# Performance work log

Hardware: AMD Instinct MI355X
Metric: run time of the kernel (lower is better)

The kernel has to match this reference:

```python
import jax, jax.numpy as jnp
import numpy as np

NH, DH = 16, 64          # n_head, d_head
CH = NH + DH             # 80
RQ, RK, RV = 6, 2, 2
ROPE_BASE = 10000.0


def _rotary(b, cache_len):
    # b: [B, T, R, DH]; rotates the d-factor exactly as the torch Rotary module
    T = b.shape[1]
    inv_freq = (1.0 / ROPE_BASE) ** (jnp.arange(0, DH, 2, dtype=jnp.float32) / DH)
    t = jnp.arange(T, dtype=jnp.float32) + cache_len
    freqs = jnp.outer(t, inv_freq)                      # [T, DH/2]
    cos = freqs[None, :, None, :].astype(b.dtype)
    sin = jnp.sin(freqs)[None, :, None, :].astype(b.dtype)
    cos = jnp.cos(freqs)[None, :, None, :].astype(b.dtype)
    x1, x2 = jnp.split(b, 2, axis=3)
    return jnp.concatenate([x1 * cos + x2 * sin, -x1 * sin + x2 * cos], axis=3)


def setup_inputs() -> dict:
    key = jax.random.key(0)
    k1, k2, k3, k4 = jax.random.split(key, 4)
    B, T, D = 2, 2048, 1024
    x = jax.random.normal(k1, (B, T, D), dtype=jnp.float32)
    # xavier-uniform-like scale for factor projections
    s_q = float(np.sqrt(6.0 / (D + CH)))
    s_o = float(np.sqrt(6.0 / (D + D)))
    W_abq = jax.random.uniform(k2, (RQ * CH, D), minval=-s_q, maxval=s_q, dtype=jnp.float32)
    W_abkv = jax.random.uniform(k3, ((RK + RV) * CH, D), minval=-s_q, maxval=s_q, dtype=jnp.float32)
    W_o = jax.random.uniform(k4, (D, D), minval=-s_o, maxval=s_o, dtype=jnp.float32)
    return {"x": x, "W_abq": W_abq, "W_abkv": W_abkv, "W_o": W_o}


def reference(x, W_abq, W_abkv, W_o):
    B, T, D = x.shape
    # low-rank factor projections
    abq = (x @ W_abq.T).reshape(B, T, RQ, CH)
    a_q, b_q = abq[..., :NH], abq[..., NH:]            # [B,T,RQ,NH], [B,T,RQ,DH]
    abkv = (x @ W_abkv.T).reshape(B, T, RK + RV, CH)
    a_kv = abkv[..., :NH]
    b_kv = _rotary(abkv[..., NH:], cache_len=0)        # RoPE applied to K/V d-factors only
    a_k, b_k = a_kv[:, :, :RK], b_kv[:, :, :RK]
    a_v, b_v = a_kv[:, :, RK:], b_kv[:, :, RK:]
    # tensor-product reconstruction of Q/K/V
    q = jnp.einsum('btrh,btrd->bthd', a_q, b_q) / RQ
    k = jnp.einsum('btrh,btrd->bthd', a_k, b_k) / RK
    v = jnp.einsum('btrh,btrd->bthd', a_v, b_v) / RV
    # causal attention (flex_attention default scale = 1/sqrt(dh))
    scale = 1.0 / jnp.sqrt(jnp.asarray(DH, dtype=q.dtype))
    scores = jnp.einsum('bqhd,bkhd->bhqk', q, k) * scale
    causal = jnp.tril(jnp.ones((T, T), dtype=bool))
    scores = jnp.where(causal[None, None], scores, jnp.finfo(scores.dtype).min)
    attn = jax.nn.softmax(scores, axis=-1)
    y = jnp.einsum('bhqk,bkhd->bqhd', attn, v).reshape(B, T, D)
    return y @ W_o.T
```

## Files before the change

### kernel.cpp

```cpp
#include <hip/hip_runtime.h>
#include <hip/hip_bf16.h>
#include <math.h>

#define NHEADS 16
#define DHEAD  64
#define CHDIM  80
#define RQn    6
#define RKn    2
#define RVn    2
#define BB     2
#define TT     2048
#define DDim   1024
#define NQK    800

using frag16 = __attribute__((ext_vector_type(8))) short;
using f32x4  = __attribute__((ext_vector_type(4))) float;
using f32x16 = __attribute__((ext_vector_type(16))) float;

#define AS1(p) ((const __attribute__((address_space(1))) unsigned int*)(p))
#define AS3(p) ((__attribute__((address_space(3))) unsigned int*)(p))

static __device__ __forceinline__ unsigned short bf16_bits(float f) {
    __hip_bfloat16 h = __float2bfloat16(f);
    return *(unsigned short*)&h;
}
static __device__ __forceinline__ unsigned int pk2(float a, float b) {
    return ((unsigned int)bf16_bits(b) << 16) | (unsigned int)bf16_bits(a);
}

__global__ __launch_bounds__(256) void cvt_all(
    const float* __restrict__ x, const float* __restrict__ wq,
    const float* __restrict__ wk, const float* __restrict__ wo,
    __hip_bfloat16* __restrict__ xb, __hip_bfloat16* __restrict__ wqk,
    __hip_bfloat16* __restrict__ wob)
{
    int bid = blockIdx.x;
    const float* src; __hip_bfloat16* dst; int n4;
    if (bid < 4096)      { src = x;  dst = xb;            n4 = 1048576; }
    else if (bid < 4576) { bid -= 4096; src = wq; dst = wqk;           n4 = 122880; }
    else if (bid < 4896) { bid -= 4576; src = wk; dst = wqk + 491520;  n4 = 81920; }
    else                 { bid -= 4896; src = wo; dst = wob;           n4 = 262144; }
    int i = bid * 256 + threadIdx.x;
    if (i < n4) {
        float4 v = *(const float4*)&src[i * 4];
        ushort4 o;
        o.x = bf16_bits(v.x); o.y = bf16_bits(v.y);
        o.z = bf16_bits(v.z); o.w = bf16_bits(v.w);
        *(ushort4*)&dst[i * 4] = o;
    }
}

__global__ __launch_bounds__(256) void gemm_bf16(
    const __hip_bfloat16* __restrict__ A, const __hip_bfloat16* __restrict__ W,
    float* __restrict__ C, int M, int N, int K)
{
    __shared__ __hip_bfloat16 Asl[2][64 * 64];
    __shared__ __hip_bfloat16 Bsl[2][128 * 64];
    const int tid = threadIdx.x;
    const int w = tid >> 6, lane = tid & 63;
    const int l16 = lane & 15, quad = lane >> 4;
    const int bm = blockIdx.y * 64, bn = blockIdx.x * 128;

    int rSA[2], cSA[2];
    #pragma unroll
    for (int j = 0; j < 2; j++) {
        int L = (w * 2 + j) * 64 + lane;
        rSA[j] = L >> 3;
        cSA[j] = (L & 7) ^ (rSA[j] & 7);
    }
    int rSB[4], cSB[4];
    #pragma unroll
    for (int j = 0; j < 4; j++) {
        int L = (w * 4 + j) * 64 + lane;
        int r = L >> 3;
        cSB[j] = (L & 7) ^ (r & 7);
        int rb = bn + r;
        rSB[j] = (rb < N) ? rb : (N - 1);
    }

    f32x4 acc[4][2];
    #pragma unroll
    for (int mt = 0; mt < 4; mt++)
        #pragma unroll
        for (int nt = 0; nt < 2; nt++)
            acc[mt][nt] = (f32x4){0.f, 0.f, 0.f, 0.f};

    const int nK = K >> 6;
    #pragma unroll
    for (int j = 0; j < 2; j++)
        __builtin_amdgcn_global_load_lds(AS1(A + (size_t)(bm + rSA[j]) * K + cSA[j] * 8),
                                         AS3(&Asl[0][(w * 2 + j) * 512]), 16, 0, 0);
    #pragma unroll
    for (int j = 0; j < 4; j++)
        __builtin_amdgcn_global_load_lds(AS1(W + (size_t)rSB[j] * K + cSB[j] * 8),
                                         AS3(&Bsl[0][(w * 4 + j) * 512]), 16, 0, 0);

    for (int kk = 0; kk < nK; kk++) {
        const int cur = kk & 1;
        __syncthreads();
        if (kk + 1 < nK) {
            const int k1 = (kk + 1) * 64;
            #pragma unroll
            for (int j = 0; j < 2; j++)
                __builtin_amdgcn_global_load_lds(AS1(A + (size_t)(bm + rSA[j]) * K + k1 + cSA[j] * 8),
                                                 AS3(&Asl[cur ^ 1][(w * 2 + j) * 512]), 16, 0, 0);
            #pragma unroll
            for (int j = 0; j < 4; j++)
                __builtin_amdgcn_global_load_lds(AS1(W + (size_t)rSB[j] * K + k1 + cSB[j] * 8),
                                                 AS3(&Bsl[cur ^ 1][(w * 4 + j) * 512]), 16, 0, 0);
        }
        #pragma unroll
        for (int ks = 0; ks < 2; ks++) {
            frag16 af[4], bf[2];
            #pragma unroll
            for (int mt = 0; mt < 4; mt++) {
                int r = mt * 16 + l16;
                af[mt] = *(const frag16*)&Asl[cur][r * 64 + (((ks * 4 + quad) ^ (r & 7)) * 8)];
            }
            #pragma unroll
            for (int nt = 0; nt < 2; nt++) {
                int r = w * 32 + nt * 16 + l16;
                bf[nt] = *(const frag16*)&Bsl[cur][r * 64 + (((ks * 4 + quad) ^ (r & 7)) * 8)];
            }
            #pragma unroll
            for (int mt = 0; mt < 4; mt++)
                #pragma unroll
                for (int nt = 0; nt < 2; nt++)
                    acc[mt][nt] = __builtin_amdgcn_mfma_f32_16x16x32_bf16(af[mt], bf[nt], acc[mt][nt], 0, 0, 0);
        }
    }
    #pragma unroll
    for (int mt = 0; mt < 4; mt++) {
        #pragma unroll
        for (int reg = 0; reg < 4; reg++) {
            int row = bm + mt * 16 + quad * 4 + reg;
            #pragma unroll
            for (int nt = 0; nt < 2; nt++) {
                int col = bn + w * 32 + nt * 16 + l16;
                if (col < N) C[(size_t)row * N + col] = acc[mt][nt][reg];
            }
        }
    }
}

__global__ __launch_bounds__(256) void qkv_kernel(
    const float* __restrict__ ab,
    __hip_bfloat16* __restrict__ q, __hip_bfloat16* __restrict__ k,
    __hip_bfloat16* __restrict__ vT)
{
    const int tok0 = blockIdx.x * 4;
    const int w = threadIdx.x >> 6;
    const int d = threadIdx.x & 63;
    const int token = tok0 + w;
    const int b = token / TT;
    const int t = token % TT;
    __shared__ float sq[4][RQn * CHDIM];
    __shared__ float skv[4][(RKn + RVn) * CHDIM];
    __shared__ __align__(8) __hip_bfloat16 vbuf[NHEADS][DHEAD][4];
    const float* aq  = ab + (size_t)token * NQK;
    const float* akv = aq + 480;
    for (int i = d; i < RQn * CHDIM; i += 64) sq[w][i] = aq[i];
    for (int i = d; i < (RKn + RVn) * CHDIM; i += 64) skv[w][i] = akv[i];
    const int i32 = d & 31;
    float inv_freq = powf(10000.0f, -(float)i32 / 32.0f);
    float fr = (float)t * inv_freq;
    float c = cosf(fr), s = sinf(fr);
    float rot[4];
    #pragma unroll
    for (int r = 0; r < 4; r++) {
        float x1 = skv[w][r * CHDIM + NHEADS + i32];
        float x2 = skv[w][r * CHDIM + NHEADS + 32 + i32];
        rot[r] = (d < 32) ? (x1 * c + x2 * s) : (-x1 * s + x2 * c);
    }
    float bqv[RQn];
    #pragma unroll
    for (int r = 0; r < RQn; r++) bqv[r] = sq[w][r * CHDIM + NHEADS + d];
    #pragma unroll
    for (int h = 0; h < NHEADS; h++) {
        float accq = 0.0f;
        #pragma unroll
        for (int r = 0; r < RQn; r++)
            accq += sq[w][r * CHDIM + h] * bqv[r];
        q[((size_t)(b * NHEADS + h) * TT + t) * DHEAD + d] = __float2bfloat16(accq * (0.125f / 6.0f));
        float acck = 0.0f, accv = 0.0f;
        #pragma unroll
        for (int r = 0; r < RKn; r++)
            acck += skv[w][r * CHDIM + h] * rot[r];
        #pragma unroll
        for (int r = 0; r < RVn; r++)
            accv += skv[w][(RKn + r) * CHDIM + h] * rot[RKn + r];
        k[((size_t)(b * NHEADS + h) * TT + t) * DHEAD + d] = __float2bfloat16(acck * 0.5f);
        vbuf[h][d][w] = __float2bfloat16(accv * 0.5f);
    }
    __syncthreads();
    const int t0 = tok0 % TT;
    const int b0 = tok0 / TT;
    for (int row = threadIdx.x; row < NHEADS * DHEAD; row += 256) {
        int h = row >> 6, dd = row & 63;
        *(uint2*)&vT[((size_t)(b0 * NHEADS + h) * DHEAD + dd) * TT + t0] =
            *(const uint2*)&vbuf[h][dd][0];
    }
}

static __device__ __forceinline__ void build_pfrag(
    const float* s0, const float* s1, frag16 Pf[4], const int hi, const int paddr)
{
    #pragma unroll
    for (int k2 = 0; k2 < 4; k2++) {
        const float* sF = (k2 >= 2) ? s1 : s0;
        const int bs = 8 * (k2 & 1);
        unsigned int u0a = pk2(sF[bs + 0], sF[bs + 1]);
        unsigned int u0b = pk2(sF[bs + 2], sF[bs + 3]);
        unsigned int u1a = pk2(sF[bs + 4], sF[bs + 5]);
        unsigned int u1b = pk2(sF[bs + 6], sF[bs + 7]);
        unsigned int r0a = (unsigned int)__builtin_amdgcn_ds_bpermute(paddr, (int)u0a);
        unsigned int r0b = (unsigned int)__builtin_amdgcn_ds_bpermute(paddr, (int)u0b);
        unsigned int r1a = (unsigned int)__builtin_amdgcn_ds_bpermute(paddr, (int)u1a);
        unsigned int r1b = (unsigned int)__builtin_amdgcn_ds_bpermute(paddr, (int)u1b);
        union { frag16 f; unsigned int u[4]; } pf;
        pf.u[0] = hi ? r1a : u0a;
        pf.u[1] = hi ? r1b : u0b;
        pf.u[2] = hi ? u1a : r0a;
        pf.u[3] = hi ? u1b : r0b;
        Pf[k2] = pf.f;
    }
}

static __device__ __forceinline__ void attn_tile(
    const __hip_bfloat16* __restrict__ Kc, const __hip_bfloat16* __restrict__ Vc,
    const frag16 qB[4], f32x16& O0, f32x16& O1, float& lpart,
    const int l31, const int hi, const int xi, const int paddr,
    const bool domask, const int kb0, const int qlane)
{
    f32x16 ST0 = {}, ST1 = {};
    #pragma unroll
    for (int kt4 = 0; kt4 < 4; kt4++) {
        int c8 = kt4 * 2 + hi;
        frag16 kf0 = *(const frag16*)&Kc[l31 * 64 + ((c8 ^ xi) * 8)];
        frag16 kf1 = *(const frag16*)&Kc[(32 + l31) * 64 + ((c8 ^ xi) * 8)];
        ST0 = __builtin_amdgcn_mfma_f32_32x32x16_bf16(kf0, qB[kt4], ST0, 0, 0, 0);
        ST1 = __builtin_amdgcn_mfma_f32_32x32x16_bf16(kf1, qB[kt4], ST1, 0, 0, 0);
    }
    float* s0 = (float*)&ST0;
    float* s1 = (float*)&ST1;
    if (domask) {
        int kbq = kb0 + 4 * hi;
        #pragma unroll
        for (int reg = 0; reg < 16; reg++) {
            int rowc = (reg & 3) + 8 * (reg >> 2);
            if (kbq + rowc > qlane)      s0[reg] = -1e30f;
            if (kbq + 32 + rowc > qlane) s1[reg] = -1e30f;
        }
    }
    #pragma unroll
    for (int reg = 0; reg < 16; reg++) {
        float p0 = __expf(s0[reg]);
        float p1 = __expf(s1[reg]);
        s0[reg] = p0; s1[reg] = p1;
        lpart += p0 + p1;
    }
    frag16 Pf[4];
    build_pfrag(s0, s1, Pf, hi, paddr);
    #pragma unroll
    for (int k2 = 0; k2 < 4; k2++) {
        int c8 = k2 * 2 + hi;
        frag16 vf0 = *(const frag16*)&Vc[l31 * 64 + ((c8 ^ xi) * 8)];
        frag16 vf1 = *(const frag16*)&Vc[(32 + l31) * 64 + ((c8 ^ xi) * 8)];
        O0 = __builtin_amdgcn_mfma_f32_32x32x16_bf16(vf0, Pf[k2], O0, 0, 0, 0);
        O1 = __builtin_amdgcn_mfma_f32_32x32x16_bf16(vf1, Pf[k2], O1, 0, 0, 0);
    }
}

static __device__ __forceinline__ void attn_tile2(
    const __hip_bfloat16* __restrict__ Kc, const __hip_bfloat16* __restrict__ Vc,
    const frag16 qBlo[4], const frag16 qBhi[4],
    f32x16& Olo0, f32x16& Olo1, float& l_lo,
    f32x16& Ohi0, f32x16& Ohi1, float& l_hi,
    const int l31, const int hi, const int xi, const int paddr,
    const bool domask_lo, const int kb0, const int qlane_lo)
{
    f32x16 SL0 = {}, SL1 = {}, SH0 = {}, SH1 = {};
    #pragma unroll
    for (int kt4 = 0; kt4 < 4; kt4++) {
        int c8 = kt4 * 2 + hi;
        frag16 kf0 = *(const frag16*)&Kc[l31 * 64 + ((c8 ^ xi) * 8)];
        frag16 kf1 = *(const frag16*)&Kc[(32 + l31) * 64 + ((c8 ^ xi) * 8)];
        SL0 = __builtin_amdgcn_mfma_f32_32x32x16_bf16(kf0, qBlo[kt4], SL0, 0, 0, 0);
        SH0 = __builtin_amdgcn_mfma_f32_32x32x16_bf16(kf0, qBhi[kt4], SH0, 0, 0, 0);
        SL1 = __builtin_amdgcn_mfma_f32_32x32x16_bf16(kf1, qBlo[kt4], SL1, 0, 0, 0);
        SH1 = __builtin_amdgcn_mfma_f32_32x32x16_bf16(kf1, qBhi[kt4], SH1, 0, 0, 0);
    }
    float* sl0 = (float*)&SL0; float* sl1 = (float*)&SL1;
    float* sh0 = (float*)&SH0; float* sh1 = (float*)&SH1;
    if (domask_lo) {
        int kbq = kb0 + 4 * hi;
        #pragma unroll
        for (int reg = 0; reg < 16; reg++) {
            int rowc = (reg & 3) + 8 * (reg >> 2);
            if (kbq + rowc > qlane_lo)      sl0[reg] = -1e30f;
            if (kbq + 32 + rowc > qlane_lo) sl1[reg] = -1e30f;
        }
    }
    #pragma unroll
    for (int reg = 0; reg < 16; reg++) {
        float a = __expf(sl0[reg]); float b = __expf(sl1[reg]);
        float c = __expf(sh0[reg]); float d = __expf(sh1[reg]);
        sl0[reg] = a; sl1[reg] = b; sh0[reg] = c; sh1[reg] = d;
        l_lo += a + b; l_hi += c + d;
    }
    frag16 PfL[4], PfH[4];
    build_pfrag(sl0, sl1, PfL, hi, paddr);
    build_pfrag(sh0, sh1, PfH, hi, paddr);
    #pragma unroll
    for (int k2 = 0; k2 < 4; k2++) {
        int c8 = k2 * 2 + hi;
        frag16 vf0 = *(const frag16*)&Vc[l31 * 64 + ((c8 ^ xi) * 8)];
        frag16 vf1 = *(const frag16*)&Vc[(32 + l31) * 64 + ((c8 ^ xi) * 8)];
        Olo0 = __builtin_amdgcn_mfma_f32_32x32x16_bf16(vf0, PfL[k2], Olo0, 0, 0, 0);
        Ohi0 = __builtin_amdgcn_mfma_f32_32x32x16_bf16(vf0, PfH[k2], Ohi0, 0, 0, 0);
        Olo1 = __builtin_amdgcn_mfma_f32_32x32x16_bf16(vf1, PfL[k2], Olo1, 0, 0, 0);
        Ohi1 = __builtin_amdgcn_mfma_f32_32x32x16_bf16(vf1, PfH[k2], Ohi1, 0, 0, 0);
    }
}

__global__ __launch_bounds__(256, 2) void flash_mfma(
    const __hip_bfloat16* __restrict__ q, const __hip_bfloat16* __restrict__ k,
    const __hip_bfloat16* __restrict__ vT, __hip_bfloat16* __restrict__ y,
    float* __restrict__ Op, float* __restrict__ Lp)
{
    const int g = blockIdx.x;
    const int bh = g & 31;
    const int pr = g >> 5;
    const int qthalf = pr & 7;
    const int part = pr >> 3;
    const int qt_lo = qthalf, qt_hi = 15 - qthalf;
    const int nlo = 2 * qt_lo + 2;
    const int S = 17 - nlo;
    const int b = bh >> 4, h = bh & 15;
    const int tid = threadIdx.x;
    const int w = tid >> 6;
    const int lane = tid & 63;
    const int l31 = lane & 31;
    const int hi = lane >> 5;
    const int xi = l31 & 7;
    const int paddr = (lane ^ 32) << 2;

    __shared__ __align__(16) __hip_bfloat16 KsF[2][4096];
    __shared__ __align__(16) __hip_bfloat16 VsF[2][4096];

    const size_t base = (size_t)bh * TT * DHEAD;
    const __hip_bfloat16* qb = q + base;
    const __hip_bfloat16* kb = k + base;
    const __hip_bfloat16* vb = vT + base;

    const int ktd_lo = 2 * qt_lo + (w >> 1);
    const int ktd_hi = 2 * qt_hi + (w >> 1);
    const int qlane_lo = qt_lo * 128 + w * 32 + l31;
    const int qlane_hi = qt_hi * 128 + w * 32 + l31;

    const int k0off  = part ? S : 0;
    const int nsteps = part ? 17 : ((nlo > S) ? nlo : S);

    int offK[2], offV[2];
    #pragma unroll
    for (int j = 0; j < 2; j++) {
        int Lc = w * 128 + j * 64 + lane;
        int r = Lc >> 3, c8 = Lc & 7, g8 = c8 ^ (r & 7);
        offK[j] = r * 64 + g8 * 8;
        offV[j] = r * TT + g8 * 8;
    }

    frag16 qB_hi[4], qB_lo[4];
    #pragma unroll
    for (int kt4 = 0; kt4 < 4; kt4++)
        qB_hi[kt4] = *(const frag16*)&qb[(size_t)qlane_hi * DHEAD + kt4 * 16 + hi * 8];
    if (part == 0) {
        #pragma unroll
        for (int kt4 = 0; kt4 < 4; kt4++)
            qB_lo[kt4] = *(const frag16*)&qb[(size_t)qlane_lo * DHEAD + kt4 * 16 + hi * 8];
    }

    f32x16 Olo0 = {}, Olo1 = {}, Ohi0 = {}, Ohi1 = {};
    float l_lo = 0.0f, l_hi = 0.0f;

    #pragma unroll
    for (int j = 0; j < 2; j++) {
        __builtin_amdgcn_global_load_lds(AS1(kb + (size_t)k0off * 4096 + offK[j]),
                                         AS3(&KsF[0][w * 1024 + j * 512]), 16, 0, 0);
        __builtin_amdgcn_global_load_lds(AS1(vb + (size_t)k0off * 64 + offV[j]),
                                         AS3(&VsF[0][w * 1024 + j * 512]), 16, 0, 0);
    }

    for (int kt = 0; kt < nsteps; kt++) {
        const int cur = kt & 1;
        __syncthreads();
        if (kt + 1 < nsteps) {
            const int phys1 = k0off + kt + 1;
            #pragma unroll
            for (int j = 0; j < 2; j++) {
                __builtin_amdgcn_global_load_lds(AS1(kb + (size_t)phys1 * 4096 + offK[j]),
                                                 AS3(&KsF[cur ^ 1][w * 1024 + j * 512]), 16, 0, 0);
                __builtin_amdgcn_global_load_lds(AS1(vb + (size_t)phys1 * 64 + offV[j]),
                                                 AS3(&VsF[cur ^ 1][w * 1024 + j * 512]), 16, 0, 0);
            }
        }
        const __hip_bfloat16* Kc = KsF[cur];
        const __hip_bfloat16* Vc = VsF[cur];
        if (part == 0) {
            const bool do_lo = (kt <= ktd_lo);
            const bool do_hi = (kt < S);
            if (do_lo && do_hi)
                attn_tile2(Kc, Vc, qB_lo, qB_hi, Olo0, Olo1, l_lo, Ohi0, Ohi1, l_hi,
                           l31, hi, xi, paddr, kt == ktd_lo, kt * 64, qlane_lo);
            else if (do_lo)
                attn_tile(Kc, Vc, qB_lo, Olo0, Olo1, l_lo, l31, hi, xi, paddr,
                          kt == ktd_lo, kt * 64, qlane_lo);
            else if (do_hi)
                attn_tile(Kc, Vc, qB_hi, Ohi0, Ohi1, l_hi, l31, hi, xi, paddr,
                          false, 0, qlane_hi);
        } else {
            const int phys = S + kt;
            if (phys <= ktd_hi)
                attn_tile(Kc, Vc, qB_hi, Ohi0, Ohi1, l_hi, l31, hi, xi, paddr,
                          phys == ktd_hi, phys * 64, qlane_hi);
        }
    }

    if (part == 0) {
        float lother = __int_as_float(__builtin_amdgcn_ds_bpermute(paddr, __float_as_int(l_lo)));
        float inv = 1.0f / (l_lo + lother);
        float* o0 = (float*)&Olo0;
        float* o1 = (float*)&Olo1;
        __hip_bfloat16* yp = y + ((size_t)(b * TT + qlane_lo)) * DDim + h * DHEAD;
        #pragma unroll
        for (int gg = 0; gg < 4; gg++) {
            int d0 = 8 * gg + 4 * hi;
            uint2 pa, pb;
            pa.x = pk2(o0[4*gg+0] * inv, o0[4*gg+1] * inv);
            pa.y = pk2(o0[4*gg+2] * inv, o0[4*gg+3] * inv);
            pb.x = pk2(o1[4*gg+0] * inv, o1[4*gg+1] * inv);
            pb.y = pk2(o1[4*gg+2] * inv, o1[4*gg+3] * inv);
            *(uint2*)&yp[d0] = pa;
            *(uint2*)&yp[32 + d0] = pb;
        }
    }
    {
        float lother = __int_as_float(__builtin_amdgcn_ds_bpermute(paddr, __float_as_int(l_hi)));
        float ltot = l_hi + lother;
        const int slot = bh * 8 + qthalf;
        const int rloc = w * 32 + l31;
        float* Od = Op + ((size_t)part * 256 + slot) * 8192 + (size_t)rloc * 64;
        float* o0 = (float*)&Ohi0;
        float* o1 = (float*)&Ohi1;
        #pragma unroll
        for (int gg = 0; gg < 4; gg++) {
            int d0 = 8 * gg + 4 * hi;
            *(float4*)&Od[d0]      = (float4){o0[4*gg+0], o0[4*gg+1], o0[4*gg+2], o0[4*gg+3]};
            *(float4*)&Od[32 + d0] = (float4){o1[4*gg+0], o1[4*gg+1], o1[4*gg+2], o1[4*gg+3]};
        }
        if (hi == 0) Lp[part * 32768 + slot * 128 + rloc] = ltot;
    }
}

__global__ __launch_bounds__(256) void combine(
    const float* __restrict__ Op, const float* __restrict__ Lp,
    __hip_bfloat16* __restrict__ y)
{
    int idx = blockIdx.x * 256 + threadIdx.x;
    int slot = idx >> 7, row = idx & 127;
    int bh = slot >> 3, qthalf = slot & 7;
    int b = bh >> 4, h = bh & 15;
    int qrow = (15 - qthalf) * 128 + row;
    float l0 = Lp[slot * 128 + row];
    float l1 = Lp[32768 + slot * 128 + row];
    float inv = 1.0f / (l0 + l1);
    const float* p0 = Op + (size_t)(slot * 128 + row) * 64;
    const float* p1 = p0 + 2097152;
    __hip_bfloat16* yp = y + ((size_t)(b * TT + qrow)) * DDim + h * DHEAD;
    #pragma unroll
    for (int c = 0; c < 64; c += 8) {
        float4 a0 = *(const float4*)&p0[c];
        float4 a1 = *(const float4*)&p0[c + 4];
        float4 b0 = *(const float4*)&p1[c];
        float4 b1 = *(const float4*)&p1[c + 4];
        uint4 o;
        o.x = pk2((a0.x + b0.x) * inv, (a0.y + b0.y) * inv);
        o.y = pk2((a0.z + b0.z) * inv, (a0.w + b0.w) * inv);
        o.z = pk2((a1.x + b1.x) * inv, (a1.y + b1.y) * inv);
        o.w = pk2((a1.z + b1.z) * inv, (a1.w + b1.w) * inv);
        *(uint4*)&yp[c] = o;
    }
}

extern "C" void kernel_launch(void* const* d_in, const int* in_sizes, int n_in,
                              void* d_out, int out_size, void* d_ws, size_t ws_size,
                              hipStream_t stream) {
    const float* x      = (const float*)d_in[0];
    const float* W_abq  = (const float*)d_in[1];
    const float* W_abkv = (const float*)d_in[2];
    const float* W_o    = (const float*)d_in[3];
    float* out = (float*)d_out;

    char* ws = (char*)d_ws;
    __hip_bfloat16* xb   = (__hip_bfloat16*)ws;  ws += (size_t)4194304 * 2;
    __hip_bfloat16* wqk  = (__hip_bfloat16*)ws;  ws += (size_t)NQK * 1024 * 2;
    __hip_bfloat16* wo_b = (__hip_bfloat16*)ws;  ws += (size_t)1048576 * 2;
    float* abqkv = (float*)ws;                   ws += (size_t)4096 * NQK * 4;
    __hip_bfloat16* qb = (__hip_bfloat16*)ws;    ws += (size_t)4194304 * 2;
    __hip_bfloat16* kb = (__hip_bfloat16*)ws;    ws += (size_t)4194304 * 2;
    __hip_bfloat16* vT = (__hip_bfloat16*)ws;    ws += (size_t)4194304 * 2;
    __hip_bfloat16* yb = (__hip_bfloat16*)ws;    ws += (size_t)4194304 * 2;
    float* Op = (float*)ws;                      ws += (size_t)2 * 2097152 * 4;
    float* Lp = (float*)ws;                      ws += (size_t)2 * 32768 * 4;

    cvt_all<<<dim3(5920), dim3(256), 0, stream>>>(x, W_abq, W_abkv, W_o, xb, wqk, wo_b);
    gemm_bf16<<<dim3(7, 64), dim3(256), 0, stream>>>(xb, wqk, abqkv, 4096, NQK, 1024);
    qkv_kernel<<<dim3(1024), dim3(256), 0, stream>>>(abqkv, qb, kb, vT);
    flash_mfma<<<dim3(512), dim3(256), 0, stream>>>(qb, kb, vT, yb, Op, Lp);
    combine<<<dim3(128), dim3(256), 0, stream>>>(Op, Lp, yb);
    gemm_bf16<<<dim3(8, 64), dim3(256), 0, stream>>>(yb, wo_b, out, 4096, 1024, 1024);
}
```

Before: 176.7 us.

## Fuse convert, QKV projection GEMM and QKV build into persistent kernel with grid barriers

Merges the conversion, first GEMM and QKV reconstruction kernels into one persistent 512-block kernel separated by atomic-counter grid barriers, with a memset to reset the counters each call. This removes two kernel launches and their inter-kernel gaps. It also removes the dual-tile attention path in flash_mfma, so the lo and hi query tiles are processed by separate attn_tile calls. The grid barrier relies on all 512 blocks being co-resident, uses system-scope fences and spinning, and adds a memset launch.

```diff
diff --git a/kernel.cpp b/kernel.cpp
--- a/kernel.cpp
+++ b/kernel.cpp
@@ -8,10 +8,10 @@
 #define RQn    6
 #define RKn    2
 #define RVn    2
-#define BB     2
 #define TT     2048
 #define DDim   1024
 #define NQK    800
+#define GRID   512
 
 using frag16 = __attribute__((ext_vector_type(8))) short;
 using f32x4  = __attribute__((ext_vector_type(4))) float;
@@ -28,26 +28,205 @@
     return ((unsigned int)bf16_bits(b) << 16) | (unsigned int)bf16_bits(a);
 }
 
-__global__ __launch_bounds__(256) void cvt_all(
+static __device__ __forceinline__ void gbar(unsigned* cell) {
+    __syncthreads();
+    if (threadIdx.x == 0) {
+        __builtin_amdgcn_s_waitcnt(0);
+        __threadfence_system();
+        __builtin_amdgcn_s_waitcnt(0);
+        __hip_atomic_fetch_add(cell, 1u, __ATOMIC_SEQ_CST, __HIP_MEMORY_SCOPE_SYSTEM);
+        while (__hip_atomic_load(cell, __ATOMIC_SEQ_CST, __HIP_MEMORY_SCOPE_SYSTEM) < (unsigned)GRID)
+            __builtin_amdgcn_s_sleep(2);
+        __threadfence_system();
+        __builtin_amdgcn_s_waitcnt(0);
+    }
+    __syncthreads();
+}
+
+static __device__ void dev_gemm(const __hip_bfloat16* __restrict__ A,
+                                const __hip_bfloat16* __restrict__ W,
+                                float* __restrict__ C,
+                                int N, int K, int bm, int bn, char* smem)
+{
+    __hip_bfloat16* Asl = (__hip_bfloat16*)smem;
+    __hip_bfloat16* Bsl = (__hip_bfloat16*)(smem + 16384);
+    const int tid = threadIdx.x;
+    const int w = tid >> 6, lane = tid & 63;
+    const int l16 = lane & 15, quad = lane >> 4;
+
+    int rSA[2], cSA[2];
+    #pragma unroll
+    for (int j = 0; j < 2; j++) {
+        int L = (w * 2 + j) * 64 + lane;
+        rSA[j] = L >> 3;
+        cSA[j] = (L & 7) ^ (rSA[j] & 7);
+    }
+    int rSB[4], cSB[4];
+    #pragma unroll
+    for (int j = 0; j < 4; j++) {
+        int L = (w * 4 + j) * 64 + lane;
+        int r = L >> 3;
+        cSB[j] = (L & 7) ^ (r & 7);
+        int rb = bn + r;
+        rSB[j] = (rb < N) ? rb : (N - 1);
+    }
+
+    f32x4 acc[4][2];
+    #pragma unroll
+    for (int mt = 0; mt < 4; mt++)
+        #pragma unroll
+        for (int nt = 0; nt < 2; nt++)
+            acc[mt][nt] = (f32x4){0.f, 0.f, 0.f, 0.f};
+
+    const int nK = K >> 6;
+    #pragma unroll
+    for (int j = 0; j < 2; j++)
+        __builtin_amdgcn_global_load_lds(AS1(A + (size_t)(bm + rSA[j]) * K + cSA[j] * 8),
+                                         AS3(&Asl[(w * 2 + j) * 512]), 16, 0, 0);
+    #pragma unroll
+    for (int j = 0; j < 4; j++)
+        __builtin_amdgcn_global_load_lds(AS1(W + (size_t)rSB[j] * K + cSB[j] * 8),
+                                         AS3(&Bsl[(w * 4 + j) * 512]), 16, 0, 0);
+
+    for (int kk = 0; kk < nK; kk++) {
+        const int cur = kk & 1;
+        __syncthreads();
+        if (kk + 1 < nK) {
+            const int k1 = (kk + 1) * 64;
+            #pragma unroll
+            for (int j = 0; j < 2; j++)
+                __builtin_amdgcn_global_load_lds(AS1(A + (size_t)(bm + rSA[j]) * K + k1 + cSA[j] * 8),
+                                                 AS3(&Asl[(cur ^ 1) * 4096 + (w * 2 + j) * 512]), 16, 0, 0);
+            #pragma unroll
+            for (int j = 0; j < 4; j++)
+                __builtin_amdgcn_global_load_lds(AS1(W + (size_t)rSB[j] * K + k1 + cSB[j] * 8),
+                                                 AS3(&Bsl[(cur ^ 1) * 8192 + (w * 4 + j) * 512]), 16, 0, 0);
+        }
+        #pragma unroll
+        for (int ks = 0; ks < 2; ks++) {
+            frag16 af[4], bf[2];
+            #pragma unroll
+            for (int mt = 0; mt < 4; mt++) {
+                int r = mt * 16 + l16;
+                af[mt] = *(const frag16*)&Asl[cur * 4096 + r * 64 + (((ks * 4 + quad) ^ (r & 7)) * 8)];
+            }
+            #pragma unroll
+            for (int nt = 0; nt < 2; nt++) {
+                int r = w * 32 + nt * 16 + l16;
+                bf[nt] = *(const frag16*)&Bsl[cur * 8192 + r * 64 + (((ks * 4 + quad) ^ (r & 7)) * 8)];
+            }
+            #pragma unroll
+            for (int mt = 0; mt < 4; mt++)
+                #pragma unroll
+                for (int nt = 0; nt < 2; nt++)
+                    acc[mt][nt] = __builtin_amdgcn_mfma_f32_16x16x32_bf16(af[mt], bf[nt], acc[mt][nt], 0, 0, 0);
+        }
+    }
+    #pragma unroll
+    for (int mt = 0; mt < 4; mt++) {
+        #pragma unroll
+        for (int reg = 0; reg < 4; reg++) {
+            int row = bm + mt * 16 + quad * 4 + reg;
+            #pragma unroll
+            for (int nt = 0; nt < 2; nt++) {
+                int col = bn + w * 32 + nt * 16 + l16;
+                if (col < N) C[(size_t)row * N + col] = acc[mt][nt][reg];
+            }
+        }
+    }
+}
+
+static __device__ void dev_qkv(const float* __restrict__ ab,
+                               __hip_bfloat16* __restrict__ q, __hip_bfloat16* __restrict__ k,
+                               __hip_bfloat16* __restrict__ vT, int vb, char* smem)
+{
+    float* sq  = (float*)smem;
+    float* skv = (float*)(smem + 7680);
+    __hip_bfloat16* vbuf = (__hip_bfloat16*)(smem + 12800);
+    __syncthreads();
+    const int tok0 = vb * 4;
+    const int w = threadIdx.x >> 6;
+    const int d = threadIdx.x & 63;
+    const int token = tok0 + w;
+    const int b = token / TT;
+    const int t = token % TT;
+    const float* aq  = ab + (size_t)token * NQK;
+    const float* akv = aq + 480;
+    for (int i = d; i < RQn * CHDIM; i += 64) sq[w * 480 + i] = aq[i];
+    for (int i = d; i < (RKn + RVn) * CHDIM; i += 64) skv[w * 320 + i] = akv[i];
+    const int i32 = d & 31;
+    float inv_freq = powf(10000.0f, -(float)i32 / 32.0f);
+    float fr = (float)t * inv_freq;
+    float c = cosf(fr), s = sinf(fr);
+    float rot[4];
+    #pragma unroll
+    for (int r = 0; r < 4; r++) {
+        float x1 = skv[w * 320 + r * CHDIM + NHEADS + i32];
+        float x2 = skv[w * 320 + r * CHDIM + NHEADS + 32 + i32];
+        rot[r] = (d < 32) ? (x1 * c + x2 * s) : (-x1 * s + x2 * c);
+    }
+    float bqv[RQn];
+    #pragma unroll
+    for (int r = 0; r < RQn; r++) bqv[r] = sq[w * 480 + r * CHDIM + NHEADS + d];
+    #pragma unroll
+    for (int h = 0; h < NHEADS; h++) {
+        float accq = 0.0f;
+        #pragma unroll
+        for (int r = 0; r < RQn; r++)
+            accq += sq[w * 480 + r * CHDIM + h] * bqv[r];
+        q[((size_t)(b * NHEADS + h) * TT + t) * DHEAD + d] = __float2bfloat16(accq * (0.125f / 6.0f));
+        float acck = 0.0f, accv = 0.0f;
+        #pragma unroll
+        for (int r = 0; r < RKn; r++)
+            acck += skv[w * 320 + r * CHDIM + h] * rot[r];
+        #pragma unroll
+        for (int r = 0; r < RVn; r++)
+            accv += skv[w * 320 + (RKn + r) * CHDIM + h] * rot[RKn + r];
+        k[((size_t)(b * NHEADS + h) * TT + t) * DHEAD + d] = __float2bfloat16(acck * 0.5f);
+        vbuf[(h * 64 + d) * 4 + w] = __float2bfloat16(accv * 0.5f);
+    }
+    __syncthreads();
+    const int t0 = tok0 % TT;
+    const int b0 = tok0 / TT;
+    for (int row = threadIdx.x; row < NHEADS * DHEAD; row += 256) {
+        int h = row >> 6, dd = row & 63;
+        *(uint2*)&vT[((size_t)(b0 * NHEADS + h) * DHEAD + dd) * TT + t0] =
+            *(const uint2*)&vbuf[(h * 64 + dd) * 4];
+    }
+}
+
+__global__ __launch_bounds__(256, 2) void front(
     const float* __restrict__ x, const float* __restrict__ wq,
     const float* __restrict__ wk, const float* __restrict__ wo,
     __hip_bfloat16* __restrict__ xb, __hip_bfloat16* __restrict__ wqk,
-    __hip_bfloat16* __restrict__ wob)
-{
-    int bid = blockIdx.x;
-    const float* src; __hip_bfloat16* dst; int n4;
-    if (bid < 4096)      { src = x;  dst = xb;            n4 = 1048576; }
-    else if (bid < 4576) { bid -= 4096; src = wq; dst = wqk;           n4 = 122880; }
-    else if (bid < 4896) { bid -= 4576; src = wk; dst = wqk + 491520;  n4 = 81920; }
-    else                 { bid -= 4896; src = wo; dst = wob;           n4 = 262144; }
-    int i = bid * 256 + threadIdx.x;
-    if (i < n4) {
-        float4 v = *(const float4*)&src[i * 4];
+    __hip_bfloat16* __restrict__ wob, float* __restrict__ abqkv,
+    __hip_bfloat16* __restrict__ qb, __hip_bfloat16* __restrict__ kb,
+    __hip_bfloat16* __restrict__ vT, unsigned* __restrict__ cnt)
+{
+    __shared__ __align__(16) char smem[49152];
+    const int g = blockIdx.x;
+    const int tid = threadIdx.x;
+
+    for (int i = g * 256 + tid; i < 1515520; i += GRID * 256) {
+        const float* src; __hip_bfloat16* dst; int off;
+        if (i < 1048576)      { src = x;  dst = xb;           off = i; }
+        else if (i < 1171456) { src = wq; dst = wqk;          off = i - 1048576; }
+        else if (i < 1253376) { src = wk; dst = wqk + 491520; off = i - 1171456; }
+        else                  { src = wo; dst = wob;          off = i - 1253376; }
+        float4 v = *(const float4*)&src[(size_t)off * 4];
         ushort4 o;
         o.x = bf16_bits(v.x); o.y = bf16_bits(v.y);
         o.z = bf16_bits(v.z); o.w = bf16_bits(v.w);
-        *(ushort4*)&dst[i * 4] = o;
-    }
+        *(ushort4*)&dst[(size_t)off * 4] = o;
+    }
+    gbar(&cnt[0]);
+
+    if (g < 448)
+        dev_gemm(xb, wqk, abqkv, NQK, 1024, (g / 7) * 64, (g % 7) * 128, smem);
+    gbar(&cnt[1]);
+
+    dev_qkv(abqkv, qb, kb, vT, g * 2 + 0, smem);
+    dev_qkv(abqkv, qb, kb, vT, g * 2 + 1, smem);
 }
 
 __global__ __launch_bounds__(256) void gemm_bf16(
@@ -140,65 +319,6 @@
                 if (col < N) C[(size_t)row * N + col] = acc[mt][nt][reg];
             }
         }
-    }
-}
-
-__global__ __launch_bounds__(256) void qkv_kernel(
-    const float* __restrict__ ab,
-    __hip_bfloat16* __restrict__ q, __hip_bfloat16* __restrict__ k,
-    __hip_bfloat16* __restrict__ vT)
-{
-    const int tok0 = blockIdx.x * 4;
-    const int w = threadIdx.x >> 6;
-    const int d = threadIdx.x & 63;
-    const int token = tok0 + w;
-    const int b = token / TT;
-    const int t = token % TT;
-    __shared__ float sq[4][RQn * CHDIM];
-    __shared__ float skv[4][(RKn + RVn) * CHDIM];
-    __shared__ __align__(8) __hip_bfloat16 vbuf[NHEADS][DHEAD][4];
-    const float* aq  = ab + (size_t)token * NQK;
-    const float* akv = aq + 480;
-    for (int i = d; i < RQn * CHDIM; i += 64) sq[w][i] = aq[i];
-    for (int i = d; i < (RKn + RVn) * CHDIM; i += 64) skv[w][i] = akv[i];
-    const int i32 = d & 31;
-    float inv_freq = powf(10000.0f, -(float)i32 / 32.0f);
-    float fr = (float)t * inv_freq;
-    float c = cosf(fr), s = sinf(fr);
-    float rot[4];
-    #pragma unroll
-    for (int r = 0; r < 4; r++) {
-        float x1 = skv[w][r * CHDIM + NHEADS + i32];
-        float x2 = skv[w][r * CHDIM + NHEADS + 32 + i32];
-        rot[r] = (d < 32) ? (x1 * c + x2 * s) : (-x1 * s + x2 * c);
-    }
-    float bqv[RQn];
-    #pragma unroll
-    for (int r = 0; r < RQn; r++) bqv[r] = sq[w][r * CHDIM + NHEADS + d];
-    #pragma unroll
-    for (int h = 0; h < NHEADS; h++) {
-        float accq = 0.0f;
-        #pragma unroll
-        for (int r = 0; r < RQn; r++)
-            accq += sq[w][r * CHDIM + h] * bqv[r];
-        q[((size_t)(b * NHEADS + h) * TT + t) * DHEAD + d] = __float2bfloat16(accq * (0.125f / 6.0f));
-        float acck = 0.0f, accv = 0.0f;
-        #pragma unroll
-        for (int r = 0; r < RKn; r++)
-            acck += skv[w][r * CHDIM + h] * rot[r];
-        #pragma unroll
-        for (int r = 0; r < RVn; r++)
-            accv += skv[w][(RKn + r) * CHDIM + h] * rot[RKn + r];
-        k[((size_t)(b * NHEADS + h) * TT + t) * DHEAD + d] = __float2bfloat16(acck * 0.5f);
-        vbuf[h][d][w] = __float2bfloat16(accv * 0.5f);
-    }
-    __syncthreads();
-    const int t0 = tok0 % TT;
-    const int b0 = tok0 / TT;
-    for (int row = threadIdx.x; row < NHEADS * DHEAD; row += 256) {
-        int h = row >> 6, dd = row & 63;
-        *(uint2*)&vT[((size_t)(b0 * NHEADS + h) * DHEAD + dd) * TT + t0] =
-            *(const uint2*)&vbuf[h][dd][0];
     }
 }
 
@@ -271,58 +391,6 @@
     }
 }
 
-static __device__ __forceinline__ void attn_tile2(
-    const __hip_bfloat16* __restrict__ Kc, const __hip_bfloat16* __restrict__ Vc,
-    const frag16 qBlo[4], const frag16 qBhi[4],
-    f32x16& Olo0, f32x16& Olo1, float& l_lo,
-    f32x16& Ohi0, f32x16& Ohi1, float& l_hi,
-    const int l31, const int hi, const int xi, const int paddr,
-    const bool domask_lo, const int kb0, const int qlane_lo)
-{
-    f32x16 SL0 = {}, SL1 = {}, SH0 = {}, SH1 = {};
-    #pragma unroll
-    for (int kt4 = 0; kt4 < 4; kt4++) {
-        int c8 = kt4 * 2 + hi;
-        frag16 kf0 = *(const frag16*)&Kc[l31 * 64 + ((c8 ^ xi) * 8)];
-        frag16 kf1 = *(const frag16*)&Kc[(32 + l31) * 64 + ((c8 ^ xi) * 8)];
-        SL0 = __builtin_amdgcn_mfma_f32_32x32x16_bf16(kf0, qBlo[kt4], SL0, 0, 0, 0);
-        SH0 = __builtin_amdgcn_mfma_f32_32x32x16_bf16(kf0, qBhi[kt4], SH0, 0, 0, 0);
-        SL1 = __builtin_amdgcn_mfma_f32_32x32x16_bf16(kf1, qBlo[kt4], SL1, 0, 0, 0);
-        SH1 = __builtin_amdgcn_mfma_f32_32x32x16_bf16(kf1, qBhi[kt4], SH1, 0, 0, 0);
-    }
-    float* sl0 = (float*)&SL0; float* sl1 = (float*)&SL1;
-    float* sh0 = (float*)&SH0; float* sh1 = (float*)&SH1;
-    if (domask_lo) {
-        int kbq = kb0 + 4 * hi;
-        #pragma unroll
-        for (int reg = 0; reg < 16; reg++) {
-            int rowc = (reg & 3) + 8 * (reg >> 2);
-            if (kbq + rowc > qlane_lo)      sl0[reg] = -1e30f;
-            if (kbq + 32 + rowc > qlane_lo) sl1[reg] = -1e30f;
-        }
-    }
-    #pragma unroll
-    for (int reg = 0; reg < 16; reg++) {
-        float a = __expf(sl0[reg]); float b = __expf(sl1[reg]);
-        float c = __expf(sh0[reg]); float d = __expf(sh1[reg]);
-        sl0[reg] = a; sl1[reg] = b; sh0[reg] = c; sh1[reg] = d;
-        l_lo += a + b; l_hi += c + d;
-    }
-    frag16 PfL[4], PfH[4];
-    build_pfrag(sl0, sl1, PfL, hi, paddr);
-    build_pfrag(sh0, sh1, PfH, hi, paddr);
-    #pragma unroll
-    for (int k2 = 0; k2 < 4; k2++) {
-        int c8 = k2 * 2 + hi;
-        frag16 vf0 = *(const frag16*)&Vc[l31 * 64 + ((c8 ^ xi) * 8)];
-        frag16 vf1 = *(const frag16*)&Vc[(32 + l31) * 64 + ((c8 ^ xi) * 8)];
-        Olo0 = __builtin_amdgcn_mfma_f32_32x32x16_bf16(vf0, PfL[k2], Olo0, 0, 0, 0);
-        Ohi0 = __builtin_amdgcn_mfma_f32_32x32x16_bf16(vf0, PfH[k2], Ohi0, 0, 0, 0);
-        Olo1 = __builtin_amdgcn_mfma_f32_32x32x16_bf16(vf1, PfL[k2], Olo1, 0, 0, 0);
-        Ohi1 = __builtin_amdgcn_mfma_f32_32x32x16_bf16(vf1, PfH[k2], Ohi1, 0, 0, 0);
-    }
-}
-
 __global__ __launch_bounds__(256, 2) void flash_mfma(
     const __hip_bfloat16* __restrict__ q, const __hip_bfloat16* __restrict__ k,
     const __hip_bfloat16* __restrict__ vT, __hip_bfloat16* __restrict__ y,
@@ -407,15 +475,10 @@
         const __hip_bfloat16* Kc = KsF[cur];
         const __hip_bfloat16* Vc = VsF[cur];
         if (part == 0) {
-            const bool do_lo = (kt <= ktd_lo);
-            const bool do_hi = (kt < S);
-            if (do_lo && do_hi)
-                attn_tile2(Kc, Vc, qB_lo, qB_hi, Olo0, Olo1, l_lo, Ohi0, Ohi1, l_hi,
-                           l31, hi, xi, paddr, kt == ktd_lo, kt * 64, qlane_lo);
-            else if (do_lo)
+            if (kt <= ktd_lo)
                 attn_tile(Kc, Vc, qB_lo, Olo0, Olo1, l_lo, l31, hi, xi, paddr,
                           kt == ktd_lo, kt * 64, qlane_lo);
-            else if (do_hi)
+            if (kt < S)
                 attn_tile(Kc, Vc, qB_hi, Ohi0, Ohi1, l_hi, l31, hi, xi, paddr,
                           false, 0, qlane_hi);
         } else {
@@ -502,6 +565,7 @@
     float* out = (float*)d_out;
 
     char* ws = (char*)d_ws;
+    unsigned* cnt = (unsigned*)ws;               ws += 256;
     __hip_bfloat16* xb   = (__hip_bfloat16*)ws;  ws += (size_t)4194304 * 2;
     __hip_bfloat16* wqk  = (__hip_bfloat16*)ws;  ws += (size_t)NQK * 1024 * 2;
     __hip_bfloat16* wo_b = (__hip_bfloat16*)ws;  ws += (size_t)1048576 * 2;
@@ -513,9 +577,9 @@
     float* Op = (float*)ws;                      ws += (size_t)2 * 2097152 * 4;
     float* Lp = (float*)ws;                      ws += (size_t)2 * 32768 * 4;
 
-    cvt_all<<<dim3(5920), dim3(256), 0, stream>>>(x, W_abq, W_abkv, W_o, xb, wqk, wo_b);
-    gemm_bf16<<<dim3(7, 64), dim3(256), 0, stream>>>(xb, wqk, abqkv, 4096, NQK, 1024);
-    qkv_kernel<<<dim3(1024), dim3(256), 0, stream>>>(abqkv, qb, kb, vT);
+    hipMemsetAsync(cnt, 0, 8 * sizeof(unsigned), stream);
+    front<<<dim3(GRID), dim3(256), 0, stream>>>(
+        x, W_abq, W_abkv, W_o, xb, wqk, wo_b, abqkv, qb, kb, vT, cnt);
     flash_mfma<<<dim3(512), dim3(256), 0, stream>>>(qb, kb, vT, yb, Op, Lp);
     combine<<<dim3(128), dim3(256), 0, stream>>>(Op, Lp, yb);
     gemm_bf16<<<dim3(8, 64), dim3(256), 0, stream>>>(yb, wo_b, out, 4096, 1024, 1024);
```

After: 323.5 us. 1.83x slower.

## Split paired causal attention work into four equal key-range parts per block

Applied to the files above, without the earlier changes.

Reorganizes the flash attention work split. Each (lo,hi) query-tile pair's 34 key steps are concatenated and divided into four roughly equal segments, one per block, giving 1024 blocks instead of 512, and the fused dual-tile path is dropped. Every partial result now goes to the Op/Lp workspace, and the combine kernel is rewritten to sum up to four partials per row, using four threads per row. Occupancy is raised to 4 blocks per CU through launch bounds. The aim is better load balance and more parallelism, at the cost of more partial-result traffic, a heavier combine, and losing the Q-fragment reuse the dual-tile path had.

```diff
diff --git a/kernel.cpp b/kernel.cpp
--- a/kernel.cpp
+++ b/kernel.cpp
@@ -8,7 +8,6 @@
 #define RQn    6
 #define RKn    2
 #define RVn    2
-#define BB     2
 #define TT     2048
 #define DDim   1024
 #define NQK    800
@@ -271,72 +270,22 @@
     }
 }
 
-static __device__ __forceinline__ void attn_tile2(
-    const __hip_bfloat16* __restrict__ Kc, const __hip_bfloat16* __restrict__ Vc,
-    const frag16 qBlo[4], const frag16 qBhi[4],
-    f32x16& Olo0, f32x16& Olo1, float& l_lo,
-    f32x16& Ohi0, f32x16& Ohi1, float& l_hi,
-    const int l31, const int hi, const int xi, const int paddr,
-    const bool domask_lo, const int kb0, const int qlane_lo)
-{
-    f32x16 SL0 = {}, SL1 = {}, SH0 = {}, SH1 = {};
-    #pragma unroll
-    for (int kt4 = 0; kt4 < 4; kt4++) {
-        int c8 = kt4 * 2 + hi;
-        frag16 kf0 = *(const frag16*)&Kc[l31 * 64 + ((c8 ^ xi) * 8)];
-        frag16 kf1 = *(const frag16*)&Kc[(32 + l31) * 64 + ((c8 ^ xi) * 8)];
-        SL0 = __builtin_amdgcn_mfma_f32_32x32x16_bf16(kf0, qBlo[kt4], SL0, 0, 0, 0);
-        SH0 = __builtin_amdgcn_mfma_f32_32x32x16_bf16(kf0, qBhi[kt4], SH0, 0, 0, 0);
-        SL1 = __builtin_amdgcn_mfma_f32_32x32x16_bf16(kf1, qBlo[kt4], SL1, 0, 0, 0);
-        SH1 = __builtin_amdgcn_mfma_f32_32x32x16_bf16(kf1, qBhi[kt4], SH1, 0, 0, 0);
-    }
-    float* sl0 = (float*)&SL0; float* sl1 = (float*)&SL1;
-    float* sh0 = (float*)&SH0; float* sh1 = (float*)&SH1;
-    if (domask_lo) {
-        int kbq = kb0 + 4 * hi;
-        #pragma unroll
-        for (int reg = 0; reg < 16; reg++) {
-            int rowc = (reg & 3) + 8 * (reg >> 2);
-            if (kbq + rowc > qlane_lo)      sl0[reg] = -1e30f;
-            if (kbq + 32 + rowc > qlane_lo) sl1[reg] = -1e30f;
-        }
-    }
-    #pragma unroll
-    for (int reg = 0; reg < 16; reg++) {
-        float a = __expf(sl0[reg]); float b = __expf(sl1[reg]);
-        float c = __expf(sh0[reg]); float d = __expf(sh1[reg]);
-        sl0[reg] = a; sl1[reg] = b; sh0[reg] = c; sh1[reg] = d;
-        l_lo += a + b; l_hi += c + d;
-    }
-    frag16 PfL[4], PfH[4];
-    build_pfrag(sl0, sl1, PfL, hi, paddr);
-    build_pfrag(sh0, sh1, PfH, hi, paddr);
-    #pragma unroll
-    for (int k2 = 0; k2 < 4; k2++) {
-        int c8 = k2 * 2 + hi;
-        frag16 vf0 = *(const frag16*)&Vc[l31 * 64 + ((c8 ^ xi) * 8)];
-        frag16 vf1 = *(const frag16*)&Vc[(32 + l31) * 64 + ((c8 ^ xi) * 8)];
-        Olo0 = __builtin_amdgcn_mfma_f32_32x32x16_bf16(vf0, PfL[k2], Olo0, 0, 0, 0);
-        Ohi0 = __builtin_amdgcn_mfma_f32_32x32x16_bf16(vf0, PfH[k2], Ohi0, 0, 0, 0);
-        Olo1 = __builtin_amdgcn_mfma_f32_32x32x16_bf16(vf1, PfL[k2], Olo1, 0, 0, 0);
-        Ohi1 = __builtin_amdgcn_mfma_f32_32x32x16_bf16(vf1, PfH[k2], Ohi1, 0, 0, 0);
-    }
-}
-
-__global__ __launch_bounds__(256, 2) void flash_mfma(
+__global__ __launch_bounds__(256, 4) void flash_mfma(
     const __hip_bfloat16* __restrict__ q, const __hip_bfloat16* __restrict__ k,
-    const __hip_bfloat16* __restrict__ vT, __hip_bfloat16* __restrict__ y,
+    const __hip_bfloat16* __restrict__ vT,
     float* __restrict__ Op, float* __restrict__ Lp)
 {
     const int g = blockIdx.x;
-    const int bh = g & 31;
-    const int pr = g >> 5;
-    const int qthalf = pr & 7;
-    const int part = pr >> 3;
+    const int part = g >> 8;
+    const int pairslot = g & 255;
+    const int bh = pairslot >> 3;
+    const int qthalf = pairslot & 7;
     const int qt_lo = qthalf, qt_hi = 15 - qthalf;
     const int nlo = 2 * qt_lo + 2;
-    const int S = 17 - nlo;
-    const int b = bh >> 4, h = bh & 15;
+    const int SB[5] = {0, 8, 17, 25, 34};
+    const int start = SB[part], end = SB[part + 1];
+    const bool hasLo = (start < nlo);
+    const bool hasHi = (end > nlo);
     const int tid = threadIdx.x;
     const int w = tid >> 6;
     const int lane = tid & 63;
@@ -358,9 +307,6 @@
     const int qlane_lo = qt_lo * 128 + w * 32 + l31;
     const int qlane_hi = qt_hi * 128 + w * 32 + l31;
 
-    const int k0off  = part ? S : 0;
-    const int nsteps = part ? 17 : ((nlo > S) ? nlo : S);
-
     int offK[2], offV[2];
     #pragma unroll
     for (int j = 0; j < 2; j++) {
@@ -370,95 +316,88 @@
         offV[j] = r * TT + g8 * 8;
     }
 
-    frag16 qB_hi[4], qB_lo[4];
-    #pragma unroll
-    for (int kt4 = 0; kt4 < 4; kt4++)
-        qB_hi[kt4] = *(const frag16*)&qb[(size_t)qlane_hi * DHEAD + kt4 * 16 + hi * 8];
-    if (part == 0) {
+    frag16 qB_lo[4], qB_hi[4];
+    if (hasLo) {
         #pragma unroll
         for (int kt4 = 0; kt4 < 4; kt4++)
             qB_lo[kt4] = *(const frag16*)&qb[(size_t)qlane_lo * DHEAD + kt4 * 16 + hi * 8];
     }
+    if (hasHi) {
+        #pragma unroll
+        for (int kt4 = 0; kt4 < 4; kt4++)
+            qB_hi[kt4] = *(const frag16*)&qb[(size_t)qlane_hi * DHEAD + kt4 * 16 + hi * 8];
+    }
 
     f32x16 Olo0 = {}, Olo1 = {}, Ohi0 = {}, Ohi1 = {};
     float l_lo = 0.0f, l_hi = 0.0f;
 
-    #pragma unroll
-    for (int j = 0; j < 2; j++) {
-        __builtin_amdgcn_global_load_lds(AS1(kb + (size_t)k0off * 4096 + offK[j]),
-                                         AS3(&KsF[0][w * 1024 + j * 512]), 16, 0, 0);
-        __builtin_amdgcn_global_load_lds(AS1(vb + (size_t)k0off * 64 + offV[j]),
-                                         AS3(&VsF[0][w * 1024 + j * 512]), 16, 0, 0);
-    }
-
-    for (int kt = 0; kt < nsteps; kt++) {
-        const int cur = kt & 1;
+    {
+        int phys0 = (start < nlo) ? start : (start - nlo);
+        #pragma unroll
+        for (int j = 0; j < 2; j++) {
+            __builtin_amdgcn_global_load_lds(AS1(kb + (size_t)phys0 * 4096 + offK[j]),
+                                             AS3(&KsF[0][w * 1024 + j * 512]), 16, 0, 0);
+            __builtin_amdgcn_global_load_lds(AS1(vb + (size_t)phys0 * 64 + offV[j]),
+                                             AS3(&VsF[0][w * 1024 + j * 512]), 16, 0, 0);
+        }
+    }
+
+    for (int ktg = start; ktg < end; ktg++) {
+        const int cur = (ktg - start) & 1;
         __syncthreads();
-        if (kt + 1 < nsteps) {
-            const int phys1 = k0off + kt + 1;
+        if (ktg + 1 < end) {
+            int pn = (ktg + 1 < nlo) ? (ktg + 1) : (ktg + 1 - nlo);
             #pragma unroll
             for (int j = 0; j < 2; j++) {
-                __builtin_amdgcn_global_load_lds(AS1(kb + (size_t)phys1 * 4096 + offK[j]),
+                __builtin_amdgcn_global_load_lds(AS1(kb + (size_t)pn * 4096 + offK[j]),
                                                  AS3(&KsF[cur ^ 1][w * 1024 + j * 512]), 16, 0, 0);
-                __builtin_amdgcn_global_load_lds(AS1(vb + (size_t)phys1 * 64 + offV[j]),
+                __builtin_amdgcn_global_load_lds(AS1(vb + (size_t)pn * 64 + offV[j]),
                                                  AS3(&VsF[cur ^ 1][w * 1024 + j * 512]), 16, 0, 0);
             }
         }
         const __hip_bfloat16* Kc = KsF[cur];
         const __hip_bfloat16* Vc = VsF[cur];
-        if (part == 0) {
-            const bool do_lo = (kt <= ktd_lo);
-            const bool do_hi = (kt < S);
-            if (do_lo && do_hi)
-                attn_tile2(Kc, Vc, qB_lo, qB_hi, Olo0, Olo1, l_lo, Ohi0, Ohi1, l_hi,
-                           l31, hi, xi, paddr, kt == ktd_lo, kt * 64, qlane_lo);
-            else if (do_lo)
+        if (ktg < nlo) {
+            int phys = ktg;
+            if (phys <= ktd_lo)
                 attn_tile(Kc, Vc, qB_lo, Olo0, Olo1, l_lo, l31, hi, xi, paddr,
-                          kt == ktd_lo, kt * 64, qlane_lo);
-            else if (do_hi)
-                attn_tile(Kc, Vc, qB_hi, Ohi0, Ohi1, l_hi, l31, hi, xi, paddr,
-                          false, 0, qlane_hi);
+                          phys == ktd_lo, phys * 64, qlane_lo);
         } else {
-            const int phys = S + kt;
+            int phys = ktg - nlo;
             if (phys <= ktd_hi)
                 attn_tile(Kc, Vc, qB_hi, Ohi0, Ohi1, l_hi, l31, hi, xi, paddr,
                           phys == ktd_hi, phys * 64, qlane_hi);
         }
     }
 
-    if (part == 0) {
+    const int rloc = w * 32 + l31;
+    if (hasLo) {
         float lother = __int_as_float(__builtin_amdgcn_ds_bpermute(paddr, __float_as_int(l_lo)));
-        float inv = 1.0f / (l_lo + lother);
+        const int slotIdx = part * 512 + pairslot * 2 + 0;
+        float* Od = Op + (size_t)slotIdx * 8192 + (size_t)rloc * 64;
         float* o0 = (float*)&Olo0;
         float* o1 = (float*)&Olo1;
-        __hip_bfloat16* yp = y + ((size_t)(b * TT + qlane_lo)) * DDim + h * DHEAD;
-        #pragma unroll
-        for (int gg = 0; gg < 4; gg++) {
-            int d0 = 8 * gg + 4 * hi;
-            uint2 pa, pb;
-            pa.x = pk2(o0[4*gg+0] * inv, o0[4*gg+1] * inv);
-            pa.y = pk2(o0[4*gg+2] * inv, o0[4*gg+3] * inv);
-            pb.x = pk2(o1[4*gg+0] * inv, o1[4*gg+1] * inv);
-            pb.y = pk2(o1[4*gg+2] * inv, o1[4*gg+3] * inv);
-            *(uint2*)&yp[d0] = pa;
-            *(uint2*)&yp[32 + d0] = pb;
-        }
-    }
-    {
-        float lother = __int_as_float(__builtin_amdgcn_ds_bpermute(paddr, __float_as_int(l_hi)));
-        float ltot = l_hi + lother;
-        const int slot = bh * 8 + qthalf;
-        const int rloc = w * 32 + l31;
-        float* Od = Op + ((size_t)part * 256 + slot) * 8192 + (size_t)rloc * 64;
-        float* o0 = (float*)&Ohi0;
-        float* o1 = (float*)&Ohi1;
         #pragma unroll
         for (int gg = 0; gg < 4; gg++) {
             int d0 = 8 * gg + 4 * hi;
             *(float4*)&Od[d0]      = (float4){o0[4*gg+0], o0[4*gg+1], o0[4*gg+2], o0[4*gg+3]};
             *(float4*)&Od[32 + d0] = (float4){o1[4*gg+0], o1[4*gg+1], o1[4*gg+2], o1[4*gg+3]};
         }
-        if (hi == 0) Lp[part * 32768 + slot * 128 + rloc] = ltot;
+        if (hi == 0) Lp[slotIdx * 128 + rloc] = l_lo + lother;
+    }
+    if (hasHi) {
+        float lother = __int_as_float(__builtin_amdgcn_ds_bpermute(paddr, __float_as_int(l_hi)));
+        const int slotIdx = part * 512 + pairslot * 2 + 1;
+        float* Od = Op + (size_t)slotIdx * 8192 + (size_t)rloc * 64;
+        float* o0 = (float*)&Ohi0;
+        float* o1 = (float*)&Ohi1;
+        #pragma unroll
+        for (int gg = 0; gg < 4; gg++) {
+            int d0 = 8 * gg + 4 * hi;
+            *(float4*)&Od[d0]      = (float4){o0[4*gg+0], o0[4*gg+1], o0[4*gg+2], o0[4*gg+3]};
+            *(float4*)&Od[32 + d0] = (float4){o1[4*gg+0], o1[4*gg+1], o1[4*gg+2], o1[4*gg+3]};
+        }
+        if (hi == 0) Lp[slotIdx * 128 + rloc] = l_hi + lother;
     }
 }
 
@@ -467,29 +406,41 @@
     __hip_bfloat16* __restrict__ y)
 {
     int idx = blockIdx.x * 256 + threadIdx.x;
-    int slot = idx >> 7, row = idx & 127;
-    int bh = slot >> 3, qthalf = slot & 7;
+    int rowid = idx >> 2, qq = idx & 3;
+    int pairslot = rowid >> 8;
+    int local = rowid & 255;
+    int seg = local >> 7, row = local & 127;
+    int bh = pairslot >> 3, qthalf = pairslot & 7;
+    int nlo = 2 * qthalf + 2;
+    int qt = seg ? (15 - qthalf) : qthalf;
     int b = bh >> 4, h = bh & 15;
-    int qrow = (15 - qthalf) * 128 + row;
-    float l0 = Lp[slot * 128 + row];
-    float l1 = Lp[32768 + slot * 128 + row];
-    float inv = 1.0f / (l0 + l1);
-    const float* p0 = Op + (size_t)(slot * 128 + row) * 64;
-    const float* p1 = p0 + 2097152;
-    __hip_bfloat16* yp = y + ((size_t)(b * TT + qrow)) * DDim + h * DHEAD;
-    #pragma unroll
-    for (int c = 0; c < 64; c += 8) {
-        float4 a0 = *(const float4*)&p0[c];
-        float4 a1 = *(const float4*)&p0[c + 4];
-        float4 b0 = *(const float4*)&p1[c];
-        float4 b1 = *(const float4*)&p1[c + 4];
-        uint4 o;
-        o.x = pk2((a0.x + b0.x) * inv, (a0.y + b0.y) * inv);
-        o.y = pk2((a0.z + b0.z) * inv, (a0.w + b0.w) * inv);
-        o.z = pk2((a1.x + b1.x) * inv, (a1.y + b1.y) * inv);
-        o.w = pk2((a1.z + b1.z) * inv, (a1.w + b1.w) * inv);
-        *(uint4*)&yp[c] = o;
-    }
+    int qrow = qt * 128 + row;
+    const int SB[5] = {0, 8, 17, 25, 34};
+    float l = 0.0f;
+    float o[16] = {};
+    #pragma unroll
+    for (int p = 0; p < 4; p++) {
+        bool use = seg ? (SB[p + 1] > nlo) : (SB[p] < nlo);
+        if (use) {
+            int slotIdx = p * 512 + pairslot * 2 + seg;
+            l += Lp[slotIdx * 128 + row];
+            const float* src = Op + (size_t)slotIdx * 8192 + (size_t)row * 64 + qq * 16;
+            #pragma unroll
+            for (int c = 0; c < 16; c += 4) {
+                float4 v = *(const float4*)&src[c];
+                o[c] += v.x; o[c+1] += v.y; o[c+2] += v.z; o[c+3] += v.w;
+            }
+        }
+    }
+    float inv = 1.0f / l;
+    __hip_bfloat16* yp = y + ((size_t)(b * TT + qrow)) * DDim + h * DHEAD + qq * 16;
+    uint4 u0, u1;
+    u0.x = pk2(o[0] * inv,  o[1] * inv);  u0.y = pk2(o[2] * inv,  o[3] * inv);
+    u0.z = pk2(o[4] * inv,  o[5] * inv);  u0.w = pk2(o[6] * inv,  o[7] * inv);
+    u1.x = pk2(o[8] * inv,  o[9] * inv);  u1.y = pk2(o[10] * inv, o[11] * inv);
+    u1.z = pk2(o[12] * inv, o[13] * inv); u1.w = pk2(o[14] * inv, o[15] * inv);
+    *(uint4*)&yp[0] = u0;
+    *(uint4*)&yp[8] = u1;
 }
 
 extern "C" void kernel_launch(void* const* d_in, const int* in_sizes, int n_in,
@@ -510,13 +461,13 @@
     __hip_bfloat16* kb = (__hip_bfloat16*)ws;    ws += (size_t)4194304 * 2;
     __hip_bfloat16* vT = (__hip_bfloat16*)ws;    ws += (size_t)4194304 * 2;
     __hip_bfloat16* yb = (__hip_bfloat16*)ws;    ws += (size_t)4194304 * 2;
-    float* Op = (float*)ws;                      ws += (size_t)2 * 2097152 * 4;
-    float* Lp = (float*)ws;                      ws += (size_t)2 * 32768 * 4;
+    float* Op = (float*)ws;                      ws += (size_t)4 * 512 * 8192 * 4;
+    float* Lp = (float*)ws;                      ws += (size_t)4 * 512 * 128 * 4;
 
     cvt_all<<<dim3(5920), dim3(256), 0, stream>>>(x, W_abq, W_abkv, W_o, xb, wqk, wo_b);
     gemm_bf16<<<dim3(7, 64), dim3(256), 0, stream>>>(xb, wqk, abqkv, 4096, NQK, 1024);
     qkv_kernel<<<dim3(1024), dim3(256), 0, stream>>>(abqkv, qb, kb, vT);
-    flash_mfma<<<dim3(512), dim3(256), 0, stream>>>(qb, kb, vT, yb, Op, Lp);
-    combine<<<dim3(128), dim3(256), 0, stream>>>(Op, Lp, yb);
+    flash_mfma<<<dim3(1024), dim3(256), 0, stream>>>(qb, kb, vT, Op, Lp);
+    combine<<<dim3(1024), dim3(256), 0, stream>>>(Op, Lp, yb);
     gemm_bf16<<<dim3(8, 64), dim3(256), 0, stream>>>(yb, wo_b, out, 4096, 1024, 1024);
 }
```

Result: slower. 355.1 us (+100.9%).
